# Performance work log

Measured on AMD Instinct MI355X. Metric: run time of the kernel, lower is better.

Reference implementation:

```python
import jax, jax.numpy as jnp
import numpy as np

B, S, H, NH = 8, 1024, 1024, 16
HD = H // NH  # 64


def _rope(x, cos, sin):
    # x: [B, NH, S, HD]; cos/sin: [1, 1, S, HD]
    x1, x2 = jnp.split(x, 2, axis=-1)
    x_rot = jnp.concatenate((-x2, x1), axis=-1)
    return x * cos + x_rot * sin


def setup_inputs() -> dict:
    key = jax.random.key(0)
    ks = jax.random.split(key, 12)
    std = 1.0 / np.sqrt(H)
    inp = {
        "hidden_states": jax.random.normal(ks[0], (B, S, H), dtype=jnp.float32),
        "cos": jax.random.uniform(ks[1], (S, HD), dtype=jnp.float32),
        "sin": jax.random.uniform(ks[2], (S, HD), dtype=jnp.float32),
        "Wq": jax.random.normal(ks[3], (H, H), dtype=jnp.float32) * std,
        "bq": jnp.zeros((H,), dtype=jnp.float32),
        "Wk": jax.random.normal(ks[4], (H, H), dtype=jnp.float32) * std,
        "bk": jnp.zeros((H,), dtype=jnp.float32),
        "Wv": jax.random.normal(ks[5], (H, H), dtype=jnp.float32) * std,
        "bv": jnp.zeros((H,), dtype=jnp.float32),
        "Wo": jax.random.normal(ks[6], (H, H), dtype=jnp.float32) * std,
        "bo": jnp.zeros((H,), dtype=jnp.float32),
    }
    return inp


def reference(hidden_states, cos, sin, Wq, bq, Wk, bk, Wv, bv, Wo, bo):
    def split_heads(t):  # [B,S,H] -> [B,NH,S,HD]
        return t.reshape(B, S, NH, HD).transpose(0, 2, 1, 3)

    q = split_heads(hidden_states @ Wq.T + bq)
    k = split_heads(hidden_states @ Wk.T + bk)
    v = split_heads(hidden_states @ Wv.T + bv)

    c = cos.reshape(1, 1, S, HD)
    s = sin.reshape(1, 1, S, HD)
    q = _rope(q, c, s)
    k = _rope(k, c, s)

    scale = 1.0 / jnp.sqrt(jnp.asarray(HD, dtype=q.dtype))
    scores = jnp.einsum("bhqd,bhkd->bhqk", q, k) * scale
    attn = jax.nn.softmax(scores, axis=-1)
    out = jnp.einsum("bhqk,bhkd->bhqd", attn, v)  # [B,NH,S,HD]
    out = out.transpose(0, 2, 1, 3).reshape(B, S, H)
    return out @ Wo.T + bo
```

## Files before the change

kernel.cpp:

```cpp
#include <hip/hip_runtime.h>
#include <hip/hip_bf16.h>
#include <stdint.h>


typedef __bf16 bf16_t;
typedef __bf16 bf16x8 __attribute__((ext_vector_type(8)));
typedef __bf16 bf16x4 __attribute__((ext_vector_type(4)));
typedef float  f32x4  __attribute__((ext_vector_type(4)));
typedef float  f32x16 __attribute__((ext_vector_type(16)));
typedef uint32_t u32x4 __attribute__((ext_vector_type(4)));

typedef __attribute__((address_space(1))) const void* as1_cvp;
typedef __attribute__((address_space(3))) void* as3_vp;

__device__ __forceinline__ f32x4 mfma16(bf16x8 a, bf16x8 b, f32x4 c) {
  return __builtin_amdgcn_mfma_f32_16x16x32_bf16(a, b, c, 0, 0, 0);
}
__device__ __forceinline__ f32x16 mfma32(bf16x8 a, bf16x8 b, f32x16 c) {
  return __builtin_amdgcn_mfma_f32_32x32x16_bf16(a, b, c, 0, 0, 0);
}

__device__ __forceinline__ void gload_lds16(const bf16_t* g, bf16_t* l) {
  __builtin_amdgcn_global_load_lds((as1_cvp)g, (as3_vp)l, 16, 0, 0);
}

__device__ __forceinline__ f32x4 zero4() {
  f32x4 z = {0.f, 0.f, 0.f, 0.f};
  return z;
}

__device__ __forceinline__ uint32_t pk2(float a, float b) {
  union { bf16_t h[2]; uint32_t u; } x;
  x.h[0] = (bf16_t)a;
  x.h[1] = (bf16_t)b;
  return x.u;
}

__global__ void cvt_all(const float* __restrict__ hs, const float* __restrict__ wq,
                        const float* __restrict__ wk, const float* __restrict__ wv,
                        const float* __restrict__ wo, bf16_t* __restrict__ Xb,
                        bf16_t* __restrict__ Wqkvb, bf16_t* __restrict__ Wob) {
  const int i = blockIdx.x * 256 + threadIdx.x;
  const f32x4* src;
  bf16x4* dst;
  if (i < 2097152) {
    src = (const f32x4*)hs + i;            dst = (bf16x4*)Xb + i;
  } else if (i < 2359296) {
    src = (const f32x4*)wq + (i - 2097152); dst = (bf16x4*)Wqkvb + (i - 2097152);
  } else if (i < 2621440) {
    src = (const f32x4*)wk + (i - 2359296); dst = (bf16x4*)Wqkvb + (i - 2359296) + 262144;
  } else if (i < 2883584) {
    src = (const f32x4*)wv + (i - 2621440); dst = (bf16x4*)Wqkvb + (i - 2621440) + 524288;
  } else {
    src = (const f32x4*)wo + (i - 2883584); dst = (bf16x4*)Wob + (i - 2883584);
  }
  const f32x4 v = *src;
  bf16x4 o;
  o[0] = (bf16_t)v[0]; o[1] = (bf16_t)v[1];
  o[2] = (bf16_t)v[2]; o[3] = (bf16_t)v[3];
  *dst = o;
}

template <int MODE>
__global__ __launch_bounds__(256, 3) void gemm128(
    const bf16_t* __restrict__ A, const bf16_t* __restrict__ Bw,
    const float* __restrict__ bQ, const float* __restrict__ bK,
    const float* __restrict__ bV, const float* __restrict__ cosp,
    const float* __restrict__ sinp,
    bf16_t* __restrict__ Qb, bf16_t* __restrict__ Kb, bf16_t* __restrict__ Vtb,
    float* __restrict__ Cout) {
  __shared__ bf16_t sm[128 * 64 * 2];
  bf16_t* sA = sm;
  bf16_t* sB = sm + 128 * 64;

  const int tid = threadIdx.x;
  const int lane = tid & 63;
  const int wid = tid >> 6;
  const int l15 = lane & 15;
  const int l4 = lane >> 4;
  const int row0 = blockIdx.x * 128;
  const int col0 = blockIdx.y * 128;
  const int wr = (wid >> 1) * 64;
  const int wc = (wid & 1) * 64;

  f32x4 acc[4][4];
#pragma unroll
  for (int mi = 0; mi < 4; ++mi)
#pragma unroll
    for (int ni = 0; ni < 4; ++ni) acc[mi][ni] = zero4();

  for (int kt = 0; kt < 16; ++kt) {
    const int k0 = kt * 64;
#pragma unroll
    for (int i = 0; i < 4; ++i) {
      const int chunk = i * 256 + tid;
      const int r = chunk >> 3, cc = chunk & 7;
      const int scc = cc ^ (r & 7);
      gload_lds16(A + (size_t)(row0 + r) * 1024 + k0 + scc * 8,
                  sA + (i * 256 + wid * 64) * 8);
      gload_lds16(Bw + (size_t)(col0 + r) * 1024 + k0 + scc * 8,
                  sB + (i * 256 + wid * 64) * 8);
    }
    __syncthreads();
    __builtin_amdgcn_s_setprio(1);
#pragma unroll
    for (int ks = 0; ks < 2; ++ks) {
      bf16x8 af[4], bfv[4];
#pragma unroll
      for (int mi = 0; mi < 4; ++mi) {
        const int r = wr + mi * 16 + l15;
        af[mi] = *(const bf16x8*)(sA + r * 64 + (((ks * 4 + l4) ^ (r & 7)) << 3));
      }
#pragma unroll
      for (int ni = 0; ni < 4; ++ni) {
        const int r = wc + ni * 16 + l15;
        bfv[ni] = *(const bf16x8*)(sB + r * 64 + (((ks * 4 + l4) ^ (r & 7)) << 3));
      }
#pragma unroll
      for (int mi = 0; mi < 4; ++mi)
#pragma unroll
        for (int ni = 0; ni < 4; ++ni)
          acc[mi][ni] = mfma16(af[mi], bfv[ni], acc[mi][ni]);
    }
    __builtin_amdgcn_s_setprio(0);
    __syncthreads();
  }

  if constexpr (MODE == 0) {
    const int proj = blockIdx.y >> 3;
    const float* bias = proj == 0 ? bQ : (proj == 1 ? bK : bV);
    if (proj < 2) {
      bf16_t* dst = proj == 0 ? Qb : Kb;
      const float qs = proj == 0 ? 0.18033688011112042f : 1.0f;
      const int base = col0 & 1023;
#pragma unroll
      for (int mi = 0; mi < 4; ++mi)
#pragma unroll
        for (int nl = 0; nl < 2; ++nl) {
          const int gcL = base + wc + nl * 16 + l15;
          const int h = gcL >> 6, dL = gcL & 63;
          const float bbL = bias[gcL], bbH = bias[gcL + 32];
#pragma unroll
          for (int j = 0; j < 4; ++j) {
            const int gr = row0 + wr + mi * 16 + l4 * 4 + j;
            const int b = gr >> 10, s = gr & 1023;
            const float cL = cosp[s * 64 + dL], cH = cosp[s * 64 + dL + 32];
            const float snL = sinp[s * 64 + dL], snH = sinp[s * 64 + dL + 32];
            const float x1 = acc[mi][nl][j] + bbL;
            const float x2 = acc[mi][nl + 2][j] + bbH;
            bf16_t* p = dst + ((size_t)(b * 16 + h) * 1024 + s) * 64 + dL;
            p[0]  = (bf16_t)((x1 * cL - x2 * snL) * qs);
            p[32] = (bf16_t)((x2 * cH + x1 * snH) * qs);
          }
        }
    } else {
      bf16_t* trb = sm;
#pragma unroll
      for (int mi = 0; mi < 4; ++mi)
#pragma unroll
        for (int ni = 0; ni < 4; ++ni) {
          const int cl = wc + ni * 16 + l15;
          const float bb = bias[(col0 & 1023) + cl];
#pragma unroll
          for (int j = 0; j < 4; ++j) {
            const int rl = wr + mi * 16 + l4 * 4 + j;
            trb[cl * 128 + (((rl >> 3) ^ (cl & 7)) << 3) + (rl & 7)] =
                (bf16_t)(acc[mi][ni][j] + bb);
          }
        }
      __syncthreads();
      const int b = row0 >> 10, s0 = row0 & 1023;
#pragma unroll
      for (int i = 0; i < 8; ++i) {
        const int chunk = i * 256 + tid;
        const int cl = chunk >> 4, rc = chunk & 15;
        const u32x4 v = *(const u32x4*)(trb + cl * 128 + ((rc ^ (cl & 7)) << 3));
        const int cv = (col0 & 1023) + cl;
        *(u32x4*)(Vtb + ((size_t)(b * 16 + (cv >> 6)) * 64 + (cv & 63)) * 1024 +
                  s0 + rc * 8) = v;
      }
    }
  } else {
#pragma unroll
    for (int mi = 0; mi < 4; ++mi)
#pragma unroll
      for (int ni = 0; ni < 4; ++ni) {
        const int gc = col0 + wc + ni * 16 + l15;
        const float bb = bQ[gc];
#pragma unroll
        for (int j = 0; j < 4; ++j) {
          const int gr = row0 + wr + mi * 16 + l4 * 4 + j;
          Cout[(size_t)gr * 1024 + gc] = acc[mi][ni][j] + bb;
        }
      }
  }
}

__global__ __launch_bounds__(256, 2) void attn_kernel(
    const bf16_t* __restrict__ Qb, const bf16_t* __restrict__ Kb,
    const bf16_t* __restrict__ Vtb, bf16_t* __restrict__ AOb) {
  __shared__ bf16_t sm[16384];
  bf16_t* sK = sm;
  bf16_t* sV = sm + 4096;
  const int tid = threadIdx.x, lane = tid & 63, wid = tid >> 6;
  const int l31 = lane & 31, l5 = lane >> 5;
  const bool loh = (l5 == 0);

  const int bh = blockIdx.x;
  const int q0 = blockIdx.y * 256;
  const bf16_t* Qg = Qb + (size_t)bh * 65536;
  const bf16_t* Kg = Kb + (size_t)bh * 65536;
  const bf16_t* Vg = Vtb + (size_t)bh * 65536;

#pragma unroll
  for (int i = 0; i < 8; ++i) {
    const int chunk = i * 256 + tid, r = chunk >> 3, c = chunk & 7;
    *(u32x4*)(sm + r * 64 + ((c ^ (r & 7)) << 3)) =
        *(const u32x4*)(Qg + (size_t)(q0 + r) * 64 + c * 8);
  }
  __syncthreads();
  bf16x8 qf[2][4];
#pragma unroll
  for (int qb = 0; qb < 2; ++qb)
#pragma unroll
    for (int step = 0; step < 4; ++step) {
      const int r = wid * 64 + qb * 32 + l31;
      qf[qb][step] =
          *(const bf16x8*)(sm + r * 64 + (((step * 2 + l5) ^ (r & 7)) << 3));
    }
  __syncthreads();

  const int ck1 = 256 + tid;
  const int kr0 = tid >> 3, kc0 = tid & 7;
  const int kr1 = ck1 >> 3, kc1 = ck1 & 7;
  bf16_t* kd0 = sK + kr0 * 64 + ((kc0 ^ (kr0 & 7)) << 3);
  bf16_t* kd1 = sK + kr1 * 64 + ((kc1 ^ (kr1 & 7)) << 3);
  bf16_t* vd0 = sV + kr0 * 64 + ((kc0 ^ (kr0 & 7)) << 3);
  bf16_t* vd1 = sV + kr1 * 64 + ((kc1 ^ (kr1 & 7)) << 3);
  const bf16_t* ksrc0 = Kg + kr0 * 64 + kc0 * 8;
  const bf16_t* ksrc1 = Kg + kr1 * 64 + kc1 * 8;
  const bf16_t* vsrc0 = Vg + kr0 * 1024 + kc0 * 8;
  const bf16_t* vsrc1 = Vg + kr1 * 1024 + kc1 * 8;

  u32x4 kv0 = *(const u32x4*)ksrc0;
  u32x4 kv1 = *(const u32x4*)ksrc1;
  u32x4 kv2 = *(const u32x4*)vsrc0;
  u32x4 kv3 = *(const u32x4*)vsrc1;

  f32x16 accO[2][2];
#pragma unroll
  for (int qb = 0; qb < 2; ++qb)
#pragma unroll
    for (int db = 0; db < 2; ++db)
#pragma unroll
      for (int r = 0; r < 16; ++r) accO[qb][db][r] = 0.f;
  float l_p[2] = {0.f, 0.f};

  for (int kt = 0; kt < 16; ++kt) {
    *(u32x4*)kd0 = kv0;
    *(u32x4*)kd1 = kv1;
    *(u32x4*)vd0 = kv2;
    *(u32x4*)vd1 = kv3;
    __syncthreads();
    if (kt < 15) {
      kv0 = *(const u32x4*)(ksrc0 + (kt + 1) * 4096);
      kv1 = *(const u32x4*)(ksrc1 + (kt + 1) * 4096);
      kv2 = *(const u32x4*)(vsrc0 + (kt + 1) * 64);
      kv3 = *(const u32x4*)(vsrc1 + (kt + 1) * 64);
    }

#pragma unroll
    for (int kb = 0; kb < 2; ++kb) {
      bf16x8 kf[4];
#pragma unroll
      for (int step = 0; step < 4; ++step) {
        const int r = kb * 32 + l31;
        kf[step] =
            *(const bf16x8*)(sK + r * 64 + (((step * 2 + l5) ^ (r & 7)) << 3));
      }
      f32x16 st0, st1;
#pragma unroll
      for (int r = 0; r < 16; ++r) { st0[r] = 0.f; st1[r] = 0.f; }
      __builtin_amdgcn_s_setprio(1);
#pragma unroll
      for (int step = 0; step < 4; ++step)
        st0 = mfma32(kf[step], qf[0][step], st0);
#pragma unroll
      for (int step = 0; step < 4; ++step)
        st1 = mfma32(kf[step], qf[1][step], st1);
      __builtin_amdgcn_s_setprio(0);

      float p0[16], p1[16];
      float rs0 = 0.f, rs1 = 0.f;
#pragma unroll
      for (int r = 0; r < 16; ++r) {
        p0[r] = __builtin_amdgcn_exp2f(st0[r]);
        rs0 += p0[r];
        p1[r] = __builtin_amdgcn_exp2f(st1[r]);
        rs1 += p1[r];
      }
      l_p[0] += rs0;
      l_p[1] += rs1;

#pragma unroll
      for (int cb = 0; cb < 2; ++cb) {
        const int c = kb * 2 + cb;
        const uint32_t A0q0 = pk2(p0[8 * cb + 0], p0[8 * cb + 1]);
        const uint32_t B0q0 = pk2(p0[8 * cb + 2], p0[8 * cb + 3]);
        const uint32_t A1q0 = pk2(p0[8 * cb + 4], p0[8 * cb + 5]);
        const uint32_t B1q0 = pk2(p0[8 * cb + 6], p0[8 * cb + 7]);
        const uint32_t TAq0 = __shfl_xor(loh ? A1q0 : A0q0, 32);
        const uint32_t TBq0 = __shfl_xor(loh ? B1q0 : B0q0, 32);
        u32x4 w0;
        w0[0] = loh ? A0q0 : TAq0;
        w0[1] = loh ? B0q0 : TBq0;
        w0[2] = loh ? TAq0 : A1q0;
        w0[3] = loh ? TBq0 : B1q0;
        const bf16x8 pa0 = __builtin_bit_cast(bf16x8, w0);
        const uint32_t A0q1 = pk2(p1[8 * cb + 0], p1[8 * cb + 1]);
        const uint32_t B0q1 = pk2(p1[8 * cb + 2], p1[8 * cb + 3]);
        const uint32_t A1q1 = pk2(p1[8 * cb + 4], p1[8 * cb + 5]);
        const uint32_t B1q1 = pk2(p1[8 * cb + 6], p1[8 * cb + 7]);
        const uint32_t TAq1 = __shfl_xor(loh ? A1q1 : A0q1, 32);
        const uint32_t TBq1 = __shfl_xor(loh ? B1q1 : B0q1, 32);
        u32x4 w1;
        w1[0] = loh ? A0q1 : TAq1;
        w1[1] = loh ? B0q1 : TBq1;
        w1[2] = loh ? TAq1 : A1q1;
        w1[3] = loh ? TBq1 : B1q1;
        const bf16x8 pa1 = __builtin_bit_cast(bf16x8, w1);

        bf16x8 vf[2];
#pragma unroll
        for (int db = 0; db < 2; ++db) {
          const int d = db * 32 + l31;
          vf[db] =
              *(const bf16x8*)(sV + d * 64 + (((c * 2 + l5) ^ (d & 7)) << 3));
        }
        __builtin_amdgcn_s_setprio(1);
        accO[0][0] = mfma32(vf[0], pa0, accO[0][0]);
        accO[0][1] = mfma32(vf[1], pa0, accO[0][1]);
        accO[1][0] = mfma32(vf[0], pa1, accO[1][0]);
        accO[1][1] = mfma32(vf[1], pa1, accO[1][1]);
        __builtin_amdgcn_s_setprio(0);
      }
    }
    __syncthreads();
  }

  float li[2];
#pragma unroll
  for (int qb = 0; qb < 2; ++qb) {
    const float t = l_p[qb] + __shfl_xor(l_p[qb], 32);
    li[qb] = __builtin_amdgcn_rcpf(t);
  }

  const int b = bh >> 4, h = bh & 15;
#pragma unroll
  for (int qb = 0; qb < 2; ++qb) {
    const int s = q0 + wid * 64 + qb * 32 + l31;
    bf16_t* rowp = AOb + ((size_t)b * 1024 + s) * 1024 + h * 64;
#pragma unroll
    for (int db = 0; db < 2; ++db)
#pragma unroll
      for (int g = 0; g < 4; ++g) {
        bf16x4 o;
#pragma unroll
        for (int j = 0; j < 4; ++j)
          o[j] = (bf16_t)(accO[qb][db][g * 4 + j] * li[qb]);
        *(bf16x4*)(rowp + db * 32 + g * 8 + l5 * 4) = o;
      }
  }
}

extern "C" void kernel_launch(void* const* d_in, const int* in_sizes, int n_in,
                              void* d_out, int out_size, void* d_ws,
                              size_t ws_size, hipStream_t stream) {
  const float* hs = (const float*)d_in[0];
  const float* cs = (const float*)d_in[1];
  const float* sn = (const float*)d_in[2];
  const float* Wq = (const float*)d_in[3];
  const float* bq = (const float*)d_in[4];
  const float* Wk = (const float*)d_in[5];
  const float* bk = (const float*)d_in[6];
  const float* Wv = (const float*)d_in[7];
  const float* bv = (const float*)d_in[8];
  const float* Wo = (const float*)d_in[9];
  const float* bo = (const float*)d_in[10];
  float* out = (float*)d_out;

  char* ws = (char*)d_ws;
  bf16_t* Xb    = (bf16_t*)(ws + 0);
  bf16_t* Wqkvb = (bf16_t*)(ws + 16777216);
  bf16_t* Wob   = (bf16_t*)(ws + 23068672);
  bf16_t* Qb    = (bf16_t*)(ws + 25165824);
  bf16_t* Kb    = (bf16_t*)(ws + 41943040);
  bf16_t* Vtb   = (bf16_t*)(ws + 58720256);
  bf16_t* AOb   = (bf16_t*)(ws + 75497472);

  cvt_all<<<12288, 256, 0, stream>>>(hs, Wq, Wk, Wv, Wo, Xb, Wqkvb, Wob);
  gemm128<0><<<dim3(64, 24), 256, 0, stream>>>(Xb, Wqkvb, bq, bk, bv, cs, sn,
                                               Qb, Kb, Vtb, nullptr);
  attn_kernel<<<dim3(128, 4), 256, 0, stream>>>(Qb, Kb, Vtb, AOb);
  gemm128<1><<<dim3(64, 8), 256, 0, stream>>>(AOb, Wob, bo, nullptr, nullptr,
                                              nullptr, nullptr, nullptr,
                                              nullptr, nullptr, out);
}
```

Measured before the change: 138.4 us.

## Replace 128x128 GEMM with 256x128 triple-buffered pipelined 8-wave GEMM

```diff
diff --git a/kernel.cpp b/kernel.cpp
--- a/kernel.cpp
+++ b/kernel.cpp
@@ -62,109 +62,181 @@
 }
 
 template <int MODE>
-__global__ __launch_bounds__(256, 3) void gemm128(
+__global__ __launch_bounds__(512, 2) void gemm256p(
     const bf16_t* __restrict__ A, const bf16_t* __restrict__ Bw,
     const float* __restrict__ bQ, const float* __restrict__ bK,
     const float* __restrict__ bV, const float* __restrict__ cosp,
     const float* __restrict__ sinp,
     bf16_t* __restrict__ Qb, bf16_t* __restrict__ Kb, bf16_t* __restrict__ Vtb,
     float* __restrict__ Cout) {
-  __shared__ bf16_t sm[128 * 64 * 2];
-  bf16_t* sA = sm;
-  bf16_t* sB = sm + 128 * 64;
-
+  extern __shared__ bf16_t smem[];
   const int tid = threadIdx.x;
-  const int lane = tid & 63;
-  const int wid = tid >> 6;
-  const int l15 = lane & 15;
-  const int l4 = lane >> 4;
-  const int row0 = blockIdx.x * 128;
-  const int col0 = blockIdx.y * 128;
-  const int wr = (wid >> 1) * 64;
-  const int wc = (wid & 1) * 64;
-
-  f32x4 acc[4][4];
-#pragma unroll
-  for (int mi = 0; mi < 4; ++mi)
-#pragma unroll
-    for (int ni = 0; ni < 4; ++ni) acc[mi][ni] = zero4();
-
-  for (int kt = 0; kt < 16; ++kt) {
-    const int k0 = kt * 64;
-#pragma unroll
-    for (int i = 0; i < 4; ++i) {
-      const int chunk = i * 256 + tid;
-      const int r = chunk >> 3, cc = chunk & 7;
-      const int scc = cc ^ (r & 7);
-      gload_lds16(A + (size_t)(row0 + r) * 1024 + k0 + scc * 8,
-                  sA + (i * 256 + wid * 64) * 8);
-      gload_lds16(Bw + (size_t)(col0 + r) * 1024 + k0 + scc * 8,
-                  sB + (i * 256 + wid * 64) * 8);
-    }
-    __syncthreads();
+  const int lane = tid & 63, wid = tid >> 6;
+  const int l15 = lane & 15, l4 = lane >> 4;
+  const int wr = wid >> 2, wc = wid & 3;
+  const int row0 = blockIdx.x * 256, col0 = blockIdx.y * 128;
+  const int nrow = ((wc >> 1) << 6) + ((wc & 1) << 4);
+
+  const int rr8 = tid >> 3, cc8 = tid & 7;
+  const int scc = cc8 ^ (rr8 & 7);
+  const bf16_t* Asrc = A + (size_t)(row0 + rr8) * 1024 + scc * 8;
+  const bf16_t* Bsrc = Bw + (size_t)(col0 + rr8) * 1024 + scc * 8;
+  const int dstw = wid * 512;
+
+  const int arow = wr * 128 + l15;
+  const int brow = nrow + l15;
+  const int aswz = arow & 7, bswz = brow & 7;
+
+  f32x4 acc[8][2];
+#pragma unroll
+  for (int mi = 0; mi < 8; ++mi) {
+    acc[mi][0] = zero4();
+    acc[mi][1] = zero4();
+  }
+
+#pragma unroll
+  for (int u = 0; u < 4; ++u)
+    gload_lds16(Asrc + (size_t)u * 65536, smem + u * 4096 + dstw);
+#pragma unroll
+  for (int u = 0; u < 2; ++u)
+    gload_lds16(Bsrc + (size_t)u * 65536, smem + 16384 + u * 4096 + dstw);
+#pragma unroll
+  for (int u = 0; u < 4; ++u)
+    gload_lds16(Asrc + (size_t)u * 65536 + 64, smem + 24576 + u * 4096 + dstw);
+#pragma unroll
+  for (int u = 0; u < 2; ++u)
+    gload_lds16(Bsrc + (size_t)u * 65536 + 64,
+                smem + 24576 + 16384 + u * 4096 + dstw);
+  asm volatile("s_waitcnt vmcnt(6)" ::: "memory");
+  __builtin_amdgcn_s_barrier();
+
+  bf16_t* cb = smem;
+  bf16_t* nb = smem + 24576;
+  bf16_t* sb = smem + 49152;
+
+#pragma unroll 1
+  for (int t = 0; t < 16; ++t) {
+    const size_t kk = (size_t)(t + 2) * 64;
+    const bool st = (t < 14);
+    bf16x8 a0[4], a1[4], b0[2], b1[2];
+
+#pragma unroll
+    for (int mi = 0; mi < 4; ++mi)
+      a0[mi] = *(const bf16x8*)(cb + (arow + mi * 16) * 64 +
+                                ((l4 ^ aswz) << 3));
+#pragma unroll
+    for (int ni = 0; ni < 2; ++ni)
+      b0[ni] = *(const bf16x8*)(cb + 16384 + (brow + ni * 32) * 64 +
+                                ((l4 ^ bswz) << 3));
+    if (st) {
+      gload_lds16(Asrc + kk, sb + dstw);
+      gload_lds16(Asrc + 65536 + kk, sb + 4096 + dstw);
+    }
+    __builtin_amdgcn_s_barrier();
     __builtin_amdgcn_s_setprio(1);
 #pragma unroll
-    for (int ks = 0; ks < 2; ++ks) {
-      bf16x8 af[4], bfv[4];
-#pragma unroll
-      for (int mi = 0; mi < 4; ++mi) {
-        const int r = wr + mi * 16 + l15;
-        af[mi] = *(const bf16x8*)(sA + r * 64 + (((ks * 4 + l4) ^ (r & 7)) << 3));
-      }
-#pragma unroll
-      for (int ni = 0; ni < 4; ++ni) {
-        const int r = wc + ni * 16 + l15;
-        bfv[ni] = *(const bf16x8*)(sB + r * 64 + (((ks * 4 + l4) ^ (r & 7)) << 3));
-      }
-#pragma unroll
-      for (int mi = 0; mi < 4; ++mi)
-#pragma unroll
-        for (int ni = 0; ni < 4; ++ni)
-          acc[mi][ni] = mfma16(af[mi], bfv[ni], acc[mi][ni]);
-    }
+    for (int mi = 0; mi < 4; ++mi)
+#pragma unroll
+      for (int ni = 0; ni < 2; ++ni)
+        acc[mi][ni] = mfma16(a0[mi], b0[ni], acc[mi][ni]);
     __builtin_amdgcn_s_setprio(0);
-    __syncthreads();
+
+#pragma unroll
+    for (int mi = 0; mi < 4; ++mi)
+      a1[mi] = *(const bf16x8*)(cb + (arow + (mi + 4) * 16) * 64 +
+                                ((l4 ^ aswz) << 3));
+    if (st) {
+      gload_lds16(Asrc + 131072 + kk, sb + 8192 + dstw);
+      gload_lds16(Asrc + 196608 + kk, sb + 12288 + dstw);
+    }
+    __builtin_amdgcn_s_barrier();
+    __builtin_amdgcn_s_setprio(1);
+#pragma unroll
+    for (int mi = 0; mi < 4; ++mi)
+#pragma unroll
+      for (int ni = 0; ni < 2; ++ni)
+        acc[mi + 4][ni] = mfma16(a1[mi], b0[ni], acc[mi + 4][ni]);
+    __builtin_amdgcn_s_setprio(0);
+
+#pragma unroll
+    for (int mi = 0; mi < 4; ++mi)
+      a0[mi] = *(const bf16x8*)(cb + (arow + mi * 16) * 64 +
+                                (((4 + l4) ^ aswz) << 3));
+#pragma unroll
+    for (int ni = 0; ni < 2; ++ni)
+      b1[ni] = *(const bf16x8*)(cb + 16384 + (brow + ni * 32) * 64 +
+                                (((4 + l4) ^ bswz) << 3));
+    if (st) gload_lds16(Bsrc + kk, sb + 16384 + dstw);
+    __builtin_amdgcn_s_barrier();
+    __builtin_amdgcn_s_setprio(1);
+#pragma unroll
+    for (int mi = 0; mi < 4; ++mi)
+#pragma unroll
+      for (int ni = 0; ni < 2; ++ni)
+        acc[mi][ni] = mfma16(a0[mi], b1[ni], acc[mi][ni]);
+    __builtin_amdgcn_s_setprio(0);
+
+#pragma unroll
+    for (int mi = 0; mi < 4; ++mi)
+      a1[mi] = *(const bf16x8*)(cb + (arow + (mi + 4) * 16) * 64 +
+                                (((4 + l4) ^ aswz) << 3));
+    if (st) gload_lds16(Bsrc + 65536 + kk, sb + 20480 + dstw);
+    __builtin_amdgcn_s_barrier();
+    __builtin_amdgcn_s_setprio(1);
+#pragma unroll
+    for (int mi = 0; mi < 4; ++mi)
+#pragma unroll
+      for (int ni = 0; ni < 2; ++ni)
+        acc[mi + 4][ni] = mfma16(a1[mi], b1[ni], acc[mi + 4][ni]);
+    __builtin_amdgcn_s_setprio(0);
+
+    if (t == 14) {
+      asm volatile("s_waitcnt vmcnt(0)" ::: "memory");
+    } else if (t < 14) {
+      asm volatile("s_waitcnt vmcnt(6)" ::: "memory");
+    }
+    __builtin_amdgcn_s_barrier();
+    bf16_t* tmp = cb; cb = nb; nb = sb; sb = tmp;
   }
 
   if constexpr (MODE == 0) {
-    const int proj = blockIdx.y >> 3;
-    const float* bias = proj == 0 ? bQ : (proj == 1 ? bK : bV);
+    const int proj = col0 >> 10;
+    const int colp = col0 & 1023;
     if (proj < 2) {
+      const float* bias = proj == 0 ? bQ : bK;
       bf16_t* dst = proj == 0 ? Qb : Kb;
       const float qs = proj == 0 ? 0.18033688011112042f : 1.0f;
-      const int base = col0 & 1023;
-#pragma unroll
-      for (int mi = 0; mi < 4; ++mi)
-#pragma unroll
-        for (int nl = 0; nl < 2; ++nl) {
-          const int gcL = base + wc + nl * 16 + l15;
-          const int h = gcL >> 6, dL = gcL & 63;
-          const float bbL = bias[gcL], bbH = bias[gcL + 32];
-#pragma unroll
-          for (int j = 0; j < 4; ++j) {
-            const int gr = row0 + wr + mi * 16 + l4 * 4 + j;
-            const int b = gr >> 10, s = gr & 1023;
-            const float cL = cosp[s * 64 + dL], cH = cosp[s * 64 + dL + 32];
-            const float snL = sinp[s * 64 + dL], snH = sinp[s * 64 + dL + 32];
-            const float x1 = acc[mi][nl][j] + bbL;
-            const float x2 = acc[mi][nl + 2][j] + bbH;
-            bf16_t* p = dst + ((size_t)(b * 16 + h) * 1024 + s) * 64 + dL;
-            p[0]  = (bf16_t)((x1 * cL - x2 * snL) * qs);
-            p[32] = (bf16_t)((x2 * cH + x1 * snH) * qs);
-          }
+      const int dL = ((wc & 1) << 4) + l15;
+      const int h = (colp + nrow) >> 6;
+      const float bbL = bias[colp + nrow + l15];
+      const float bbH = bias[colp + nrow + l15 + 32];
+#pragma unroll
+      for (int mi = 0; mi < 8; ++mi)
+#pragma unroll
+        for (int j = 0; j < 4; ++j) {
+          const int gr = row0 + wr * 128 + mi * 16 + l4 * 4 + j;
+          const int b = gr >> 10, s = gr & 1023;
+          const float cL = cosp[s * 64 + dL], cH = cosp[s * 64 + dL + 32];
+          const float snL = sinp[s * 64 + dL], snH = sinp[s * 64 + dL + 32];
+          const float x1 = acc[mi][0][j] + bbL;
+          const float x2 = acc[mi][1][j] + bbH;
+          bf16_t* p = dst + ((size_t)(b * 16 + h) * 1024 + s) * 64 + dL;
+          p[0]  = (bf16_t)((x1 * cL - x2 * snL) * qs);
+          p[32] = (bf16_t)((x2 * cH + x1 * snH) * qs);
         }
     } else {
-      bf16_t* trb = sm;
-#pragma unroll
-      for (int mi = 0; mi < 4; ++mi)
-#pragma unroll
-        for (int ni = 0; ni < 4; ++ni) {
-          const int cl = wc + ni * 16 + l15;
-          const float bb = bias[(col0 & 1023) + cl];
+      __syncthreads();
+      bf16_t* trb = smem;
+#pragma unroll
+      for (int mi = 0; mi < 8; ++mi)
+#pragma unroll
+        for (int ni = 0; ni < 2; ++ni) {
+          const int cl = nrow + ni * 32 + l15;
+          const float bb = bV[colp + cl];
 #pragma unroll
           for (int j = 0; j < 4; ++j) {
-            const int rl = wr + mi * 16 + l4 * 4 + j;
-            trb[cl * 128 + (((rl >> 3) ^ (cl & 7)) << 3) + (rl & 7)] =
+            const int rl = wr * 128 + mi * 16 + l4 * 4 + j;
+            trb[cl * 256 + (((rl >> 3) ^ (cl & 7)) << 3) + (rl & 7)] =
                 (bf16_t)(acc[mi][ni][j] + bb);
           }
         }
@@ -172,24 +244,25 @@
       const int b = row0 >> 10, s0 = row0 & 1023;
 #pragma unroll
       for (int i = 0; i < 8; ++i) {
-        const int chunk = i * 256 + tid;
-        const int cl = chunk >> 4, rc = chunk & 15;
-        const u32x4 v = *(const u32x4*)(trb + cl * 128 + ((rc ^ (cl & 7)) << 3));
-        const int cv = (col0 & 1023) + cl;
+        const int chunk = i * 512 + tid;
+        const int cl = chunk >> 5, rc = chunk & 31;
+        const u32x4 v =
+            *(const u32x4*)(trb + cl * 256 + ((rc ^ (cl & 7)) << 3));
+        const int cv = colp + cl;
         *(u32x4*)(Vtb + ((size_t)(b * 16 + (cv >> 6)) * 64 + (cv & 63)) * 1024 +
                   s0 + rc * 8) = v;
       }
     }
   } else {
 #pragma unroll
-    for (int mi = 0; mi < 4; ++mi)
-#pragma unroll
-      for (int ni = 0; ni < 4; ++ni) {
-        const int gc = col0 + wc + ni * 16 + l15;
+    for (int mi = 0; mi < 8; ++mi)
+#pragma unroll
+      for (int ni = 0; ni < 2; ++ni) {
+        const int gc = col0 + nrow + ni * 32 + l15;
         const float bb = bQ[gc];
 #pragma unroll
         for (int j = 0; j < 4; ++j) {
-          const int gr = row0 + wr + mi * 16 + l4 * 4 + j;
+          const int gr = row0 + wr * 128 + mi * 16 + l4 * 4 + j;
           Cout[(size_t)gr * 1024 + gc] = acc[mi][ni][j] + bb;
         }
       }
@@ -398,11 +471,16 @@
   bf16_t* Vtb   = (bf16_t*)(ws + 58720256);
   bf16_t* AOb   = (bf16_t*)(ws + 75497472);
 
+  (void)hipFuncSetAttribute((const void*)gemm256p<0>,
+                            hipFuncAttributeMaxDynamicSharedMemorySize, 147456);
+  (void)hipFuncSetAttribute((const void*)gemm256p<1>,
+                            hipFuncAttributeMaxDynamicSharedMemorySize, 147456);
+
   cvt_all<<<12288, 256, 0, stream>>>(hs, Wq, Wk, Wv, Wo, Xb, Wqkvb, Wob);
-  gemm128<0><<<dim3(64, 24), 256, 0, stream>>>(Xb, Wqkvb, bq, bk, bv, cs, sn,
-                                               Qb, Kb, Vtb, nullptr);
+  gemm256p<0><<<dim3(32, 24), 512, 147456, stream>>>(
+      Xb, Wqkvb, bq, bk, bv, cs, sn, Qb, Kb, Vtb, nullptr);
   attn_kernel<<<dim3(128, 4), 256, 0, stream>>>(Qb, Kb, Vtb, AOb);
-  gemm128<1><<<dim3(64, 8), 256, 0, stream>>>(AOb, Wob, bo, nullptr, nullptr,
-                                              nullptr, nullptr, nullptr,
-                                              nullptr, nullptr, out);
-}
+  gemm256p<1><<<dim3(32, 8), 512, 147456, stream>>>(
+      AOb, Wob, bo, nullptr, nullptr, nullptr, nullptr, nullptr, nullptr,
+      nullptr, out);
+}
```

Measured after the change: 142.8 us. 1.03x slower.

## Halve attention query tile to raise occupancy and use permlane32_swap

Applied to the files above, without the earlier changes.

```diff
diff --git a/kernel.cpp b/kernel.cpp
--- a/kernel.cpp
+++ b/kernel.cpp
@@ -9,6 +9,7 @@
 typedef float  f32x4  __attribute__((ext_vector_type(4)));
 typedef float  f32x16 __attribute__((ext_vector_type(16)));
 typedef uint32_t u32x4 __attribute__((ext_vector_type(4)));
+typedef uint32_t u32x2 __attribute__((ext_vector_type(2)));
 
 typedef __attribute__((address_space(1))) const void* as1_cvp;
 typedef __attribute__((address_space(3))) void* as3_vp;
@@ -196,38 +197,37 @@
   }
 }
 
-__global__ __launch_bounds__(256, 2) void attn_kernel(
+__global__ __launch_bounds__(256, 4) void attn_kernel(
     const bf16_t* __restrict__ Qb, const bf16_t* __restrict__ Kb,
     const bf16_t* __restrict__ Vtb, bf16_t* __restrict__ AOb) {
-  __shared__ bf16_t sm[16384];
+  __shared__ bf16_t sm[8192];
   bf16_t* sK = sm;
   bf16_t* sV = sm + 4096;
   const int tid = threadIdx.x, lane = tid & 63, wid = tid >> 6;
   const int l31 = lane & 31, l5 = lane >> 5;
   const bool loh = (l5 == 0);
+  (void)loh;
 
   const int bh = blockIdx.x;
-  const int q0 = blockIdx.y * 256;
+  const int q0 = blockIdx.y * 128;
   const bf16_t* Qg = Qb + (size_t)bh * 65536;
   const bf16_t* Kg = Kb + (size_t)bh * 65536;
   const bf16_t* Vg = Vtb + (size_t)bh * 65536;
 
 #pragma unroll
-  for (int i = 0; i < 8; ++i) {
+  for (int i = 0; i < 4; ++i) {
     const int chunk = i * 256 + tid, r = chunk >> 3, c = chunk & 7;
     *(u32x4*)(sm + r * 64 + ((c ^ (r & 7)) << 3)) =
         *(const u32x4*)(Qg + (size_t)(q0 + r) * 64 + c * 8);
   }
   __syncthreads();
-  bf16x8 qf[2][4];
-#pragma unroll
-  for (int qb = 0; qb < 2; ++qb)
-#pragma unroll
-    for (int step = 0; step < 4; ++step) {
-      const int r = wid * 64 + qb * 32 + l31;
-      qf[qb][step] =
-          *(const bf16x8*)(sm + r * 64 + (((step * 2 + l5) ^ (r & 7)) << 3));
-    }
+  bf16x8 qf[4];
+#pragma unroll
+  for (int step = 0; step < 4; ++step) {
+    const int r = wid * 32 + l31;
+    qf[step] =
+        *(const bf16x8*)(sm + r * 64 + (((step * 2 + l5) ^ (r & 7)) << 3));
+  }
   __syncthreads();
 
   const int ck1 = 256 + tid;
@@ -247,14 +247,12 @@
   u32x4 kv2 = *(const u32x4*)vsrc0;
   u32x4 kv3 = *(const u32x4*)vsrc1;
 
-  f32x16 accO[2][2];
-#pragma unroll
-  for (int qb = 0; qb < 2; ++qb)
-#pragma unroll
-    for (int db = 0; db < 2; ++db)
-#pragma unroll
-      for (int r = 0; r < 16; ++r) accO[qb][db][r] = 0.f;
-  float l_p[2] = {0.f, 0.f};
+  f32x16 accO[2];
+#pragma unroll
+  for (int db = 0; db < 2; ++db)
+#pragma unroll
+    for (int r = 0; r < 16; ++r) accO[db][r] = 0.f;
+  float l_p = 0.f;
 
   for (int kt = 0; kt < 16; ++kt) {
     *(u32x4*)kd0 = kv0;
@@ -272,64 +270,34 @@
 #pragma unroll
     for (int kb = 0; kb < 2; ++kb) {
       bf16x8 kf[4];
-#pragma unroll
-      for (int step = 0; step < 4; ++step) {
-        const int r = kb * 32 + l31;
+      const int r = kb * 32 + l31;
+#pragma unroll
+      for (int step = 0; step < 4; ++step)
         kf[step] =
             *(const bf16x8*)(sK + r * 64 + (((step * 2 + l5) ^ (r & 7)) << 3));
-      }
-      f32x16 st0, st1;
-#pragma unroll
-      for (int r = 0; r < 16; ++r) { st0[r] = 0.f; st1[r] = 0.f; }
+      f32x16 st;
+#pragma unroll
+      for (int q = 0; q < 16; ++q) st[q] = 0.f;
       __builtin_amdgcn_s_setprio(1);
 #pragma unroll
       for (int step = 0; step < 4; ++step)
-        st0 = mfma32(kf[step], qf[0][step], st0);
-#pragma unroll
-      for (int step = 0; step < 4; ++step)
-        st1 = mfma32(kf[step], qf[1][step], st1);
+        st = mfma32(kf[step], qf[step], st);
       __builtin_amdgcn_s_setprio(0);
 
-      float p0[16], p1[16];
-      float rs0 = 0.f, rs1 = 0.f;
-#pragma unroll
-      for (int r = 0; r < 16; ++r) {
-        p0[r] = __builtin_amdgcn_exp2f(st0[r]);
-        rs0 += p0[r];
-        p1[r] = __builtin_amdgcn_exp2f(st1[r]);
-        rs1 += p1[r];
-      }
-      l_p[0] += rs0;
-      l_p[1] += rs1;
-
-#pragma unroll
-      for (int cb = 0; cb < 2; ++cb) {
-        const int c = kb * 2 + cb;
-        const uint32_t A0q0 = pk2(p0[8 * cb + 0], p0[8 * cb + 1]);
-        const uint32_t B0q0 = pk2(p0[8 * cb + 2], p0[8 * cb + 3]);
-        const uint32_t A1q0 = pk2(p0[8 * cb + 4], p0[8 * cb + 5]);
-        const uint32_t B1q0 = pk2(p0[8 * cb + 6], p0[8 * cb + 7]);
-        const uint32_t TAq0 = __shfl_xor(loh ? A1q0 : A0q0, 32);
-        const uint32_t TBq0 = __shfl_xor(loh ? B1q0 : B0q0, 32);
-        u32x4 w0;
-        w0[0] = loh ? A0q0 : TAq0;
-        w0[1] = loh ? B0q0 : TBq0;
-        w0[2] = loh ? TAq0 : A1q0;
-        w0[3] = loh ? TBq0 : B1q0;
-        const bf16x8 pa0 = __builtin_bit_cast(bf16x8, w0);
-        const uint32_t A0q1 = pk2(p1[8 * cb + 0], p1[8 * cb + 1]);
-        const uint32_t B0q1 = pk2(p1[8 * cb + 2], p1[8 * cb + 3]);
-        const uint32_t A1q1 = pk2(p1[8 * cb + 4], p1[8 * cb + 5]);
-        const uint32_t B1q1 = pk2(p1[8 * cb + 6], p1[8 * cb + 7]);
-        const uint32_t TAq1 = __shfl_xor(loh ? A1q1 : A0q1, 32);
-        const uint32_t TBq1 = __shfl_xor(loh ? B1q1 : B0q1, 32);
-        u32x4 w1;
-        w1[0] = loh ? A0q1 : TAq1;
-        w1[1] = loh ? B0q1 : TBq1;
-        w1[2] = loh ? TAq1 : A1q1;
-        w1[3] = loh ? TBq1 : B1q1;
-        const bf16x8 pa1 = __builtin_bit_cast(bf16x8, w1);
-
+      float p[16];
+      float rsa = 0.f, rsb = 0.f;
+#pragma unroll
+      for (int q = 0; q < 16; q += 2) {
+        p[q] = __builtin_amdgcn_exp2f(st[q]);
+        p[q + 1] = __builtin_amdgcn_exp2f(st[q + 1]);
+        rsa += p[q];
+        rsb += p[q + 1];
+      }
+      l_p += rsa + rsb;
+
+#pragma unroll
+      for (int cbk = 0; cbk < 2; ++cbk) {
+        const int c = kb * 2 + cbk;
         bf16x8 vf[2];
 #pragma unroll
         for (int db = 0; db < 2; ++db) {
@@ -337,40 +305,56 @@
           vf[db] =
               *(const bf16x8*)(sV + d * 64 + (((c * 2 + l5) ^ (d & 7)) << 3));
         }
+
+        const uint32_t A0 = pk2(p[8 * cbk + 0], p[8 * cbk + 1]);
+        const uint32_t B0 = pk2(p[8 * cbk + 2], p[8 * cbk + 3]);
+        const uint32_t A1 = pk2(p[8 * cbk + 4], p[8 * cbk + 5]);
+        const uint32_t B1 = pk2(p[8 * cbk + 6], p[8 * cbk + 7]);
+
+        u32x4 w;
+#if __has_builtin(__builtin_amdgcn_permlane32_swap)
+        {
+          const u32x2 ra = __builtin_amdgcn_permlane32_swap(A0, A1, false, false);
+          const u32x2 rb = __builtin_amdgcn_permlane32_swap(B0, B1, false, false);
+          w[0] = ra.x; w[1] = rb.x; w[2] = ra.y; w[3] = rb.y;
+        }
+#else
+        {
+          const uint32_t TA = __shfl_xor(loh ? A1 : A0, 32);
+          const uint32_t TB = __shfl_xor(loh ? B1 : B0, 32);
+          w[0] = loh ? A0 : TA;
+          w[1] = loh ? B0 : TB;
+          w[2] = loh ? TA : A1;
+          w[3] = loh ? TB : B1;
+        }
+#endif
+        const bf16x8 pa = __builtin_bit_cast(bf16x8, w);
+
         __builtin_amdgcn_s_setprio(1);
-        accO[0][0] = mfma32(vf[0], pa0, accO[0][0]);
-        accO[0][1] = mfma32(vf[1], pa0, accO[0][1]);
-        accO[1][0] = mfma32(vf[0], pa1, accO[1][0]);
-        accO[1][1] = mfma32(vf[1], pa1, accO[1][1]);
+        accO[0] = mfma32(vf[0], pa, accO[0]);
+        accO[1] = mfma32(vf[1], pa, accO[1]);
         __builtin_amdgcn_s_setprio(0);
       }
     }
     __syncthreads();
   }
 
-  float li[2];
-#pragma unroll
-  for (int qb = 0; qb < 2; ++qb) {
-    const float t = l_p[qb] + __shfl_xor(l_p[qb], 32);
-    li[qb] = __builtin_amdgcn_rcpf(t);
-  }
+  const float lt = l_p + __shfl_xor(l_p, 32);
+  const float li = __builtin_amdgcn_rcpf(lt);
 
   const int b = bh >> 4, h = bh & 15;
-#pragma unroll
-  for (int qb = 0; qb < 2; ++qb) {
-    const int s = q0 + wid * 64 + qb * 32 + l31;
-    bf16_t* rowp = AOb + ((size_t)b * 1024 + s) * 1024 + h * 64;
-#pragma unroll
-    for (int db = 0; db < 2; ++db)
-#pragma unroll
-      for (int g = 0; g < 4; ++g) {
-        bf16x4 o;
-#pragma unroll
-        for (int j = 0; j < 4; ++j)
-          o[j] = (bf16_t)(accO[qb][db][g * 4 + j] * li[qb]);
-        *(bf16x4*)(rowp + db * 32 + g * 8 + l5 * 4) = o;
-      }
-  }
+  const int s = q0 + wid * 32 + l31;
+  bf16_t* rowp = AOb + ((size_t)b * 1024 + s) * 1024 + h * 64;
+#pragma unroll
+  for (int db = 0; db < 2; ++db)
+#pragma unroll
+    for (int g = 0; g < 4; ++g) {
+      bf16x4 o;
+#pragma unroll
+      for (int j = 0; j < 4; ++j)
+        o[j] = (bf16_t)(accO[db][g * 4 + j] * li);
+      *(bf16x4*)(rowp + db * 32 + g * 8 + l5 * 4) = o;
+    }
 }
 
 extern "C" void kernel_launch(void* const* d_in, const int* in_sizes, int n_in,
@@ -401,7 +385,7 @@
   cvt_all<<<12288, 256, 0, stream>>>(hs, Wq, Wk, Wv, Wo, Xb, Wqkvb, Wob);
   gemm128<0><<<dim3(64, 24), 256, 0, stream>>>(Xb, Wqkvb, bq, bk, bv, cs, sn,
                                                Qb, Kb, Vtb, nullptr);
-  attn_kernel<<<dim3(128, 4), 256, 0, stream>>>(Qb, Kb, Vtb, AOb);
+  attn_kernel<<<dim3(128, 8), 256, 0, stream>>>(Qb, Kb, Vtb, AOb);
   gemm128<1><<<dim3(64, 8), 256, 0, stream>>>(AOb, Wob, bo, nullptr, nullptr,
                                               nullptr, nullptr, nullptr,
                                               nullptr, nullptr, out);
```

Result: no change. 136.0 us (-1.7%).
